# Optimization experiments

Measured on AMD Instinct MI355X. Metric: run time of the kernel, lower is better.

## Reference

```python
import jax, jax.numpy as jnp
import numpy as np

B, T, K = 512, 1024, 48          # batch, seq_len, n_tokens
START, END = 46, 47              # token_dict['START'], token_dict['END']
NEG = -10000.0


def setup_inputs() -> dict:
    key = jax.random.key(0)
    k1, k2 = jax.random.split(key)
    feats = jax.random.normal(k1, (B, T, K), dtype=jnp.float32)
    transitions = jax.random.normal(k2, (K, K), dtype=jnp.float32)
    return {"feats": feats, "transitions": transitions}


def _mask_transitions(transitions):
    # Mirrors __init__: no transition out of END-column target / into START row.
    t = transitions.at[START, :].set(NEG)
    t = t.at[:, END].set(NEG)
    return t


def _crf_logz(feats, trans):
    """forward_prop: CRF forward algorithm. feats [T,K], trans [K_next,K_prev]."""
    init = jnp.full((K,), NEG, feats.dtype).at[START].set(0.0)

    def step(alpha, feat):
        # scores[next, prev] = alpha[prev] + trans[next, prev] + feat[next]
        scores = alpha[None, :] + trans + feat[:, None]
        return jax.nn.logsumexp(scores, axis=1), None

    alpha, _ = jax.lax.scan(step, init, feats)
    return jax.nn.logsumexp(alpha + trans[END])


def _viterbi(feats, trans):
    """viterbi_decode: max-product recurrence + backtrace. feats [T,K]."""
    init = jnp.full((K,), NEG, feats.dtype).at[START].set(0.0)

    def step(v, feat):
        # NOTE: original takes argmax BEFORE adding emission, then adds feat.
        scores = v[None, :] + trans          # [K_next, K_prev]
        bp = jnp.argmax(scores, axis=1)      # backpointers [K]
        return jnp.max(scores, axis=1) + feat, bp

    v, bptrs = jax.lax.scan(step, init, feats)   # bptrs [T, K]
    term = v + trans[END]
    last = jnp.argmax(term)
    path_score = term[last]

    def back(tag, bp):
        return bp[tag], tag

    _, path = jax.lax.scan(back, last, bptrs, reverse=True)  # path [T]
    return path_score, path


def reference(feats, transitions):
    trans = _mask_transitions(transitions)
    logz = jax.vmap(lambda f: _crf_logz(f, trans))(feats)          # [B]
    scores, paths = jax.vmap(lambda f: _viterbi(f, trans))(feats)  # [B], [B,T]
    return logz, scores, paths
```

## Files before the change

### kernel.cpp

```cpp
#include <hip/hip_runtime.h>

#define NB 512
#define NT 1024
#define NK 48
#define NEGV -10000.0f
#define S_START 46
#define S_END 47
#define NCH 64
#define CLEN 16

__device__ __forceinline__ float rfl_f32(float x) {
    return __int_as_float(__builtin_amdgcn_readfirstlane(__float_as_int(x)));
}

extern "C" __global__ __launch_bounds__(256, 1)
void crf_fused(const float* __restrict__ feats, const float* __restrict__ trans,
               float* __restrict__ out)
{
    __shared__ unsigned char bp[NT * NK];
    __shared__ float ckpt[4 * NK];
    __shared__ unsigned char comp[NCH * NK];
    __shared__ unsigned char boundary[NCH];
    __shared__ float eabuf[64];
    __shared__ float vbuf1[64];
    __shared__ float vbufw[2][64];

    const int b = blockIdx.x;
    const int wave = threadIdx.x >> 6;
    const int lane = threadIdx.x & 63;
    const bool act = lane < NK;
    const int LL = act ? lane : (NK - 1);
    const float* f = feats + (size_t)b * NT * NK;
    const float* fb = f + LL;

    float tEnd = NEGV;
    if (act && lane != S_END) tEnd = trans[S_END * NK + lane];

    if (wave == 0) {
        float Erow[NK];
        {
            const bool rowdead = (lane == S_START);
            const float4* r4 = (const float4*)(trans + LL * NK);
            #pragma unroll
            for (int q = 0; q < NK / 4; ++q) {
                float4 r = r4[q];
                const int c = 4 * q;
                Erow[c + 0] = (rowdead || c + 0 == S_END) ? 0.0f : __expf(r.x);
                Erow[c + 1] = (rowdead || c + 1 == S_END) ? 0.0f : __expf(r.y);
                Erow[c + 2] = (rowdead || c + 2 == S_END) ? 0.0f : __expf(r.z);
                Erow[c + 3] = (rowdead || c + 3 == S_END) ? 0.0f : __expf(r.w);
            }
        }
        float u = (lane == S_START) ? 0.0f : NEGV;
        float Muni = 0.0f;
        eabuf[lane] = __expf(u);
        __builtin_amdgcn_wave_barrier();
        float fr0 = fb[0 * NK], fr1 = fb[1 * NK], fr2 = fb[2 * NK], fr3 = fb[3 * NK];

        auto fstep = [&](float fc) {
            float ea[NK];
            {
                const float4* e4 = (const float4*)eabuf;
                #pragma unroll
                for (int q = 0; q < NK / 4; ++q) {
                    float4 r = e4[q];
                    ea[4 * q + 0] = r.x; ea[4 * q + 1] = r.y;
                    ea[4 * q + 2] = r.z; ea[4 * q + 3] = r.w;
                }
            }
            float a0 = 0.f, a1 = 0.f, a2 = 0.f, a3 = 0.f;
            #pragma unroll
            for (int p = 0; p < NK; p += 4) {
                a0 = fmaf(Erow[p + 0], ea[p + 0], a0);
                a1 = fmaf(Erow[p + 1], ea[p + 1], a1);
                a2 = fmaf(Erow[p + 2], ea[p + 2], a2);
                a3 = fmaf(Erow[p + 3], ea[p + 3], a3);
            }
            float acc = (a0 + a1) + (a2 + a3);
            float w = __logf(acc) + fc;
            float dM = rfl_f32(w);
            Muni += dM;
            u = w - dM;
            __builtin_amdgcn_wave_barrier();
            eabuf[lane] = __expf(u);
            __builtin_amdgcn_wave_barrier();
        };

        __syncthreads();
        for (int it = 0; it <= NCH; ++it) {
            if (it < NCH) {
                #pragma unroll
                for (int g = 0; g < 4; ++g) {
                    const int t = it * CLEN + 4 * g;
                    { float fc = fr0; int nr = (t + 4 < NT) ? t + 4 : NT - 1; fr0 = fb[nr * NK]; fstep(fc); }
                    { float fc = fr1; int nr = (t + 5 < NT) ? t + 5 : NT - 1; fr1 = fb[nr * NK]; fstep(fc); }
                    { float fc = fr2; int nr = (t + 6 < NT) ? t + 6 : NT - 1; fr2 = fb[nr * NK]; fstep(fc); }
                    { float fc = fr3; int nr = (t + 7 < NT) ? t + 7 : NT - 1; fr3 = fb[nr * NK]; fstep(fc); }
                }
            }
            __syncthreads();
        }
        float x = act ? (u + tEnd) : -INFINITY;
        float M2 = x;
        #pragma unroll
        for (int off = 32; off >= 1; off >>= 1)
            M2 = fmaxf(M2, __shfl_xor(M2, off, 64));
        float e = __expf(x - M2);
        #pragma unroll
        for (int off = 32; off >= 1; off >>= 1)
            e += __shfl_xor(e, off, 64);
        if (lane == 0) out[b] = Muni + M2 + __logf(e);
    } else if (wave == 1) {
        float trow[NK];
        {
            const bool rowdead = (lane == S_START);
            const float4* r4 = (const float4*)(trans + LL * NK);
            #pragma unroll
            for (int q = 0; q < NK / 4; ++q) {
                float4 r = r4[q];
                const int c = 4 * q;
                trow[c + 0] = (rowdead || c + 0 == S_END) ? NEGV : r.x;
                trow[c + 1] = (rowdead || c + 1 == S_END) ? NEGV : r.y;
                trow[c + 2] = (rowdead || c + 2 == S_END) ? NEGV : r.z;
                trow[c + 3] = (rowdead || c + 3 == S_END) ? NEGV : r.w;
            }
        }
        float v = (lane == S_START) ? 0.0f : NEGV;
        vbuf1[lane] = v;
        if (act) ckpt[0 * NK + lane] = v;
        __builtin_amdgcn_wave_barrier();
        float fr0 = fb[0 * NK], fr1 = fb[1 * NK], fr2 = fb[2 * NK], fr3 = fb[3 * NK];

        auto vstep = [&](float fc) {
            float s[NK];
            {
                const float4* v4 = (const float4*)vbuf1;
                #pragma unroll
                for (int q = 0; q < NK / 4; ++q) {
                    float4 r = v4[q];
                    s[4 * q + 0] = r.x + trow[4 * q + 0];
                    s[4 * q + 1] = r.y + trow[4 * q + 1];
                    s[4 * q + 2] = r.z + trow[4 * q + 2];
                    s[4 * q + 3] = r.w + trow[4 * q + 3];
                }
            }
            float m16[16];
            #pragma unroll
            for (int i = 0; i < 16; ++i)
                m16[i] = fmaxf(fmaxf(s[3 * i], s[3 * i + 1]), s[3 * i + 2]);
            float m6[6];
            #pragma unroll
            for (int i = 0; i < 5; ++i)
                m6[i] = fmaxf(fmaxf(m16[3 * i], m16[3 * i + 1]), m16[3 * i + 2]);
            m6[5] = m16[15];
            float best = fmaxf(fmaxf(fmaxf(m6[0], m6[1]), m6[2]),
                               fmaxf(fmaxf(m6[3], m6[4]), m6[5]));
            v = best + fc;
            __builtin_amdgcn_wave_barrier();
            vbuf1[lane] = v;
            __builtin_amdgcn_wave_barrier();
        };

        int last = 0;
        __syncthreads();
        for (int it = 0; it <= NCH; ++it) {
            if (it < NCH) {
                #pragma unroll
                for (int g = 0; g < 4; ++g) {
                    const int t = it * CLEN + 4 * g;
                    { float fc = fr0; int nr = (t + 4 < NT) ? t + 4 : NT - 1; fr0 = fb[nr * NK]; vstep(fc); }
                    { float fc = fr1; int nr = (t + 5 < NT) ? t + 5 : NT - 1; fr1 = fb[nr * NK]; vstep(fc); }
                    { float fc = fr2; int nr = (t + 6 < NT) ? t + 6 : NT - 1; fr2 = fb[nr * NK]; vstep(fc); }
                    { float fc = fr3; int nr = (t + 7 < NT) ? t + 7 : NT - 1; fr3 = fb[nr * NK]; vstep(fc); }
                }
                if (act && it + 1 < NCH) ckpt[((it + 1) & 3) * NK + lane] = v;
            } else {
                float xv = act ? (v + tEnd) : -INFINITY;
                int idx = act ? lane : 63;
                float val = xv;
                #pragma unroll
                for (int off = 32; off >= 1; off >>= 1) {
                    float ov = __shfl_xor(val, off, 64);
                    int   oi = __shfl_xor(idx, off, 64);
                    if (ov > val || (ov == val && oi < idx)) { val = ov; idx = oi; }
                }
                if (lane == 0) out[NB + b] = val;
                last = idx;
            }
            __syncthreads();
        }
        if (lane == 0) {
            int tag = last;
            for (int l = NCH - 1; l >= 0; --l) {
                boundary[l] = (unsigned char)tag;
                tag = comp[l * NK + tag];
            }
        }
        __builtin_amdgcn_wave_barrier();
        int tag = boundary[lane];
        float* pout = out + 2 * NB + (size_t)b * NT;
        const int tbase = lane * CLEN;
        for (int i = CLEN - 1; i >= 0; --i) {
            pout[tbase + i] = (float)tag;
            tag = bp[(tbase + i) * NK + tag];
        }
    } else {
        const int w = wave - 2;
        float trow[NK];
        {
            const bool rowdead = (lane == S_START);
            const float4* r4 = (const float4*)(trans + LL * NK);
            #pragma unroll
            for (int q = 0; q < NK / 4; ++q) {
                float4 r = r4[q];
                const int c = 4 * q;
                trow[c + 0] = (rowdead || c + 0 == S_END) ? NEGV : r.x;
                trow[c + 1] = (rowdead || c + 1 == S_END) ? NEGV : r.y;
                trow[c + 2] = (rowdead || c + 2 == S_END) ? NEGV : r.z;
                trow[c + 3] = (rowdead || c + 3 == S_END) ? NEGV : r.w;
            }
        }
        float* vbw = vbufw[w];
        const int big = 63;
        int bpl[8], bph[8];

        auto replay8 = [&](int c, int base, int* bparr8) {
            const float* fbc = fb + (size_t)c * CLEN * NK;
            unsigned char* bpc = bp + (size_t)c * CLEN * NK;
            float fv[8];
            #pragma unroll
            for (int i = 0; i < 8; ++i) fv[i] = fbc[(base + i) * NK];
            #pragma unroll
            for (int i = 0; i < 8; ++i) {
                float s[NK];
                {
                    const float4* v4 = (const float4*)vbw;
                    #pragma unroll
                    for (int q = 0; q < NK / 4; ++q) {
                        float4 r = v4[q];
                        s[4 * q + 0] = r.x + trow[4 * q + 0];
                        s[4 * q + 1] = r.y + trow[4 * q + 1];
                        s[4 * q + 2] = r.z + trow[4 * q + 2];
                        s[4 * q + 3] = r.w + trow[4 * q + 3];
                    }
                }
                float m16[16];
                #pragma unroll
                for (int j = 0; j < 16; ++j)
                    m16[j] = fmaxf(fmaxf(s[3 * j], s[3 * j + 1]), s[3 * j + 2]);
                float m6[6];
                #pragma unroll
                for (int j = 0; j < 5; ++j)
                    m6[j] = fmaxf(fmaxf(m16[3 * j], m16[3 * j + 1]), m16[3 * j + 2]);
                m6[5] = m16[15];
                float best = fmaxf(fmaxf(fmaxf(m6[0], m6[1]), m6[2]),
                                   fmaxf(fmaxf(m6[3], m6[4]), m6[5]));
                int ix[NK];
                #pragma unroll
                for (int p = 0; p < NK; ++p)
                    ix[p] = (s[p] != best) ? big : p;
                int n16[16];
                #pragma unroll
                for (int j = 0; j < 16; ++j)
                    n16[j] = min(min(ix[3 * j], ix[3 * j + 1]), ix[3 * j + 2]);
                int n6[6];
                #pragma unroll
                for (int j = 0; j < 5; ++j)
                    n6[j] = min(min(n16[3 * j], n16[3 * j + 1]), n16[3 * j + 2]);
                n6[5] = n16[15];
                int bi = min(min(min(n6[0], n6[1]), n6[2]),
                             min(min(n6[3], n6[4]), n6[5]));

                bparr8[i] = bi;
                bpc[(base + i) * NK + LL] = (unsigned char)bi;
                float vn = best + fv[i];
                __builtin_amdgcn_wave_barrier();
                vbw[lane] = vn;
                __builtin_amdgcn_wave_barrier();
            }
        };

        __syncthreads();
        for (int it = 0; it <= NCH; ++it) {
            if ((it & 1) == w && it < NCH) {
                vbw[lane] = ckpt[(it & 3) * NK + LL];
                __builtin_amdgcn_wave_barrier();
                replay8(it, 0, bpl);
            } else if ((it & 1) != w && it >= 1) {
                const int c = it - 1;
                replay8(c, 8, bph);
                int tag = act ? lane : 0;
                #pragma unroll
                for (int i = 7; i >= 0; --i)
                    tag = __builtin_amdgcn_ds_bpermute(tag << 2, bph[i]);
                #pragma unroll
                for (int i = 7; i >= 0; --i)
                    tag = __builtin_amdgcn_ds_bpermute(tag << 2, bpl[i]);
                if (act) comp[c * NK + lane] = (unsigned char)tag;
            }
            __syncthreads();
        }
    }
}

extern "C" void kernel_launch(void* const* d_in, const int* in_sizes, int n_in,
                              void* d_out, int out_size, void* d_ws, size_t ws_size,
                              hipStream_t stream) {
    (void)in_sizes; (void)n_in; (void)d_ws; (void)ws_size; (void)out_size;
    const float* feats = (const float*)d_in[0];
    const float* trans = (const float*)d_in[1];
    float* out = (float*)d_out;
    crf_fused<<<dim3(NB), dim3(256), 0, stream>>>(feats, trans, out);
}
```

Baseline: 495.6 us.

## Prefetch whole feature chunks and broadcast replay state via readlane

The forward and Viterbi waves now load all 16 emission values of the next chunk into registers before running the current chunk, replacing the rolling 4-deep prefetch. This gives global loads more time to arrive but uses more registers. The replay waves no longer exchange the Viterbi vector through shared memory with wave barriers. Each lane instead reads all 48 lanes' values with readlane into scalar registers, trading LDS round-trips for 48 readlane instructions per step.

```diff
diff --git a/kernel.cpp b/kernel.cpp
--- a/kernel.cpp
+++ b/kernel.cpp
@@ -11,6 +11,9 @@
 
 __device__ __forceinline__ float rfl_f32(float x) {
     return __int_as_float(__builtin_amdgcn_readfirstlane(__float_as_int(x)));
+}
+__device__ __forceinline__ float rlane_f32(float x, int k) {
+    return __int_as_float(__builtin_amdgcn_readlane(__float_as_int(x), k));
 }
 
 extern "C" __global__ __launch_bounds__(256, 1)
@@ -23,7 +26,6 @@
     __shared__ unsigned char boundary[NCH];
     __shared__ float eabuf[64];
     __shared__ float vbuf1[64];
-    __shared__ float vbufw[2][64];
 
     const int b = blockIdx.x;
     const int wave = threadIdx.x >> 6;
@@ -55,7 +57,6 @@
         float Muni = 0.0f;
         eabuf[lane] = __expf(u);
         __builtin_amdgcn_wave_barrier();
-        float fr0 = fb[0 * NK], fr1 = fb[1 * NK], fr2 = fb[2 * NK], fr3 = fb[3 * NK];
 
         auto fstep = [&](float fc) {
             float ea[NK];
@@ -86,17 +87,22 @@
             __builtin_amdgcn_wave_barrier();
         };
 
+        float fcur[CLEN], fnext[CLEN];
+        #pragma unroll
+        for (int i = 0; i < CLEN; ++i) fcur[i] = fb[i * NK];
         __syncthreads();
         for (int it = 0; it <= NCH; ++it) {
             if (it < NCH) {
                 #pragma unroll
-                for (int g = 0; g < 4; ++g) {
-                    const int t = it * CLEN + 4 * g;
-                    { float fc = fr0; int nr = (t + 4 < NT) ? t + 4 : NT - 1; fr0 = fb[nr * NK]; fstep(fc); }
-                    { float fc = fr1; int nr = (t + 5 < NT) ? t + 5 : NT - 1; fr1 = fb[nr * NK]; fstep(fc); }
-                    { float fc = fr2; int nr = (t + 6 < NT) ? t + 6 : NT - 1; fr2 = fb[nr * NK]; fstep(fc); }
-                    { float fc = fr3; int nr = (t + 7 < NT) ? t + 7 : NT - 1; fr3 = fb[nr * NK]; fstep(fc); }
-                }
+                for (int i = 0; i < CLEN; ++i) {
+                    int t = (it + 1) * CLEN + i;
+                    if (t >= NT) t = NT - 1;
+                    fnext[i] = fb[t * NK];
+                }
+                #pragma unroll
+                for (int i = 0; i < CLEN; ++i) fstep(fcur[i]);
+                #pragma unroll
+                for (int i = 0; i < CLEN; ++i) fcur[i] = fnext[i];
             }
             __syncthreads();
         }
@@ -129,7 +135,6 @@
         vbuf1[lane] = v;
         if (act) ckpt[0 * NK + lane] = v;
         __builtin_amdgcn_wave_barrier();
-        float fr0 = fb[0 * NK], fr1 = fb[1 * NK], fr2 = fb[2 * NK], fr3 = fb[3 * NK];
 
         auto vstep = [&](float fc) {
             float s[NK];
@@ -161,18 +166,23 @@
             __builtin_amdgcn_wave_barrier();
         };
 
+        float fcur[CLEN], fnext[CLEN];
+        #pragma unroll
+        for (int i = 0; i < CLEN; ++i) fcur[i] = fb[i * NK];
         int last = 0;
         __syncthreads();
         for (int it = 0; it <= NCH; ++it) {
             if (it < NCH) {
                 #pragma unroll
-                for (int g = 0; g < 4; ++g) {
-                    const int t = it * CLEN + 4 * g;
-                    { float fc = fr0; int nr = (t + 4 < NT) ? t + 4 : NT - 1; fr0 = fb[nr * NK]; vstep(fc); }
-                    { float fc = fr1; int nr = (t + 5 < NT) ? t + 5 : NT - 1; fr1 = fb[nr * NK]; vstep(fc); }
-                    { float fc = fr2; int nr = (t + 6 < NT) ? t + 6 : NT - 1; fr2 = fb[nr * NK]; vstep(fc); }
-                    { float fc = fr3; int nr = (t + 7 < NT) ? t + 7 : NT - 1; fr3 = fb[nr * NK]; vstep(fc); }
-                }
+                for (int i = 0; i < CLEN; ++i) {
+                    int t = (it + 1) * CLEN + i;
+                    if (t >= NT) t = NT - 1;
+                    fnext[i] = fb[t * NK];
+                }
+                #pragma unroll
+                for (int i = 0; i < CLEN; ++i) vstep(fcur[i]);
+                #pragma unroll
+                for (int i = 0; i < CLEN; ++i) fcur[i] = fnext[i];
                 if (act && it + 1 < NCH) ckpt[((it + 1) & 3) * NK + lane] = v;
             } else {
                 float xv = act ? (v + tEnd) : -INFINITY;
@@ -220,9 +230,9 @@
                 trow[c + 3] = (rowdead || c + 3 == S_END) ? NEGV : r.w;
             }
         }
-        float* vbw = vbufw[w];
         const int big = 63;
         int bpl[8], bph[8];
+        float vl = 0.0f;
 
         auto replay8 = [&](int c, int base, int* bparr8) {
             const float* fbc = fb + (size_t)c * CLEN * NK;
@@ -233,16 +243,12 @@
             #pragma unroll
             for (int i = 0; i < 8; ++i) {
                 float s[NK];
-                {
-                    const float4* v4 = (const float4*)vbw;
-                    #pragma unroll
-                    for (int q = 0; q < NK / 4; ++q) {
-                        float4 r = v4[q];
-                        s[4 * q + 0] = r.x + trow[4 * q + 0];
-                        s[4 * q + 1] = r.y + trow[4 * q + 1];
-                        s[4 * q + 2] = r.z + trow[4 * q + 2];
-                        s[4 * q + 3] = r.w + trow[4 * q + 3];
-                    }
+                #pragma unroll
+                for (int p = 0; p < NK; p += 4) {
+                    s[p + 0] = rlane_f32(vl, p + 0) + trow[p + 0];
+                    s[p + 1] = rlane_f32(vl, p + 1) + trow[p + 1];
+                    s[p + 2] = rlane_f32(vl, p + 2) + trow[p + 2];
+                    s[p + 3] = rlane_f32(vl, p + 3) + trow[p + 3];
                 }
                 float m16[16];
                 #pragma unroll
@@ -273,18 +279,14 @@
 
                 bparr8[i] = bi;
                 bpc[(base + i) * NK + LL] = (unsigned char)bi;
-                float vn = best + fv[i];
-                __builtin_amdgcn_wave_barrier();
-                vbw[lane] = vn;
-                __builtin_amdgcn_wave_barrier();
+                vl = best + fv[i];
             }
         };
 
         __syncthreads();
         for (int it = 0; it <= NCH; ++it) {
             if ((it & 1) == w && it < NCH) {
-                vbw[lane] = ckpt[(it & 3) * NK + LL];
-                __builtin_amdgcn_wave_barrier();
+                vl = ckpt[(it & 3) * NK + LL];
                 replay8(it, 0, bpl);
             } else if ((it & 1) != w && it >= 1) {
                 const int c = it - 1;
```

New measurement: 537.7 us. 1.08x slower.
